# Kernel tuning notes

Measured on AMD Instinct MI355X. Metric: run time of the kernel, lower is better.

## Reference

```python
import jax, jax.numpy as jnp
import numpy as np

N_EMBD = 768
N_EXP = 8
DIM_HIDDEN = int(N_EMBD * 4 * 2 / 3)  # 2048
B = 8
CAP = 1024


def setup_inputs() -> dict:
    key = jax.random.key(0)
    k1, k2, k3 = jax.random.split(key, 3)
    std_fc = N_EXP ** (-0.5)  # matches torch init: dim = c_fc.shape[0] = n_exp
    x = jax.random.normal(k1, (B, N_EXP, CAP, N_EMBD), dtype=jnp.float32)
    c_fc = jax.random.uniform(k2, (N_EXP, N_EMBD, 2 * DIM_HIDDEN), dtype=jnp.float32,
                              minval=-std_fc, maxval=std_fc)
    c_proj = jax.random.uniform(k3, (N_EXP, DIM_HIDDEN, N_EMBD), dtype=jnp.float32,
                                minval=-std_fc, maxval=std_fc)
    gamma = jnp.ones((N_EMBD,), dtype=jnp.float32)       # RMSNorm gamma
    mult_bias = jnp.ones((DIM_HIDDEN,), dtype=jnp.float32)  # GEGLU mult_bias
    return {"x": x, "c_fc": c_fc, "c_proj": c_proj, "gamma": gamma, "mult_bias": mult_bias}


def _moe_forward(x, c_fc, c_proj, gamma, mult_bias):
    # x: [b, e, n, d] -> [e, b, n, d]
    h = jnp.transpose(x, (1, 0, 2, 3))
    # RMSNorm (prenorm): F.normalize(x, dim=-1) * gamma * sqrt(d)
    scale = N_EMBD ** 0.5
    l2 = jnp.sqrt(jnp.sum(h * h, axis=-1, keepdims=True))
    h = h / jnp.maximum(l2, 1e-12) * gamma * scale
    # per-expert grouped GEMM: [e,b,n,d] @ [e,d,2h] -> [e,b,n,2h]
    u = jnp.einsum('ebnd,edh->ebnh', h, c_fc)
    # GEGLU: first half is value, second half is gate
    v, gate = u[..., :DIM_HIDDEN], u[..., DIM_HIDDEN:]
    g = jax.nn.gelu(gate, approximate=False) * v * mult_bias
    # project back: [e,b,n,h] @ [e,h,d] -> [e,b,n,d]
    out = jnp.einsum('ebnh,ehd->ebnd', g, c_proj)
    # back to [b, e, n, d]; dropout is identity (p=0.0)
    return jnp.transpose(out, (1, 0, 2, 3))


def reference(x, c_fc, c_proj, gamma, mult_bias):
    return _moe_forward(x, c_fc, c_proj, gamma, mult_bias)
```

## Files before the change

kernel.cpp:

```cpp
#include <hip/hip_runtime.h>
#include <math.h>

#define N_EMBD 768
#define N_EXP  8
#define DIMH   2048
#define CAPN   1024
#define M_TOT  8192

typedef __bf16 bf16x8 __attribute__((ext_vector_type(8)));
typedef float  f32x4  __attribute__((ext_vector_type(4)));
typedef unsigned short u16x4 __attribute__((ext_vector_type(4)));

__device__ __forceinline__ unsigned short f2bf(float f) {
    unsigned int u = __float_as_uint(f);
    unsigned int r = (u + 0x7fffu + ((u >> 16) & 1u)) >> 16;
    return (unsigned short)r;
}

__device__ __forceinline__ void gload16(const void* g, void* l) {
    __builtin_amdgcn_global_load_lds(
        (const __attribute__((address_space(1))) unsigned int*)g,
        (__attribute__((address_space(3))) unsigned int*)l, 16, 0, 0);
}

__device__ __forceinline__ float gelu_exact(float x) {
    float ax = fabsf(x);
    float z  = ax * 0.70710678118654752f;
    float t  = __builtin_amdgcn_rcpf(fmaf(0.3275911f, z, 1.0f));
    float p  = fmaf(t, 1.061405429f, -1.453152027f);
    p = fmaf(p, t, 1.421413741f);
    p = fmaf(p, t, -0.284496736f);
    p = fmaf(p, t, 0.254829592f);
    p = p * t;
    float ez = __expf(-z * z);
    float erfz = fmaf(-p, ez, 1.0f);
    return 0.5f * fmaf(ax, erfz, x);
}

__global__ __launch_bounds__(256) void norm_convert_kernel(
        const float* __restrict__ x, const float* __restrict__ gamma,
        unsigned short* __restrict__ h) {
    int r = (blockIdx.x << 2) | (threadIdx.x >> 6);
    int lane = threadIdx.x & 63;
    int e = r >> 13, m = r & 8191;
    int b = m >> 10, nc = m & 1023;
    const float4* row = (const float4*)(x + (size_t)((b * N_EXP + e) * CAPN + nc) * N_EMBD);
    const float4* g4  = (const float4*)gamma;

    float4 v0 = row[lane], v1 = row[lane + 64], v2 = row[lane + 128];
    float acc = v0.x*v0.x + v0.y*v0.y + v0.z*v0.z + v0.w*v0.w
              + v1.x*v1.x + v1.y*v1.y + v1.z*v1.z + v1.w*v1.w
              + v2.x*v2.x + v2.y*v2.y + v2.z*v2.z + v2.w*v2.w;
#pragma unroll
    for (int off = 32; off >= 1; off >>= 1) acc += __shfl_xor(acc, off, 64);
    float s = 27.712812921102035f / fmaxf(sqrtf(acc), 1e-12f);

    float4 g0 = g4[lane], g1 = g4[lane + 64], g2 = g4[lane + 128];
    u16x4* o4 = (u16x4*)(h + (size_t)(e * M_TOT + m) * N_EMBD);
    u16x4 o;
    o[0]=f2bf(v0.x*s*g0.x); o[1]=f2bf(v0.y*s*g0.y); o[2]=f2bf(v0.z*s*g0.z); o[3]=f2bf(v0.w*s*g0.w);
    o4[lane] = o;
    o[0]=f2bf(v1.x*s*g1.x); o[1]=f2bf(v1.y*s*g1.y); o[2]=f2bf(v1.z*s*g1.z); o[3]=f2bf(v1.w*s*g1.w);
    o4[lane + 64] = o;
    o[0]=f2bf(v2.x*s*g2.x); o[1]=f2bf(v2.y*s*g2.y); o[2]=f2bf(v2.z*s*g2.z); o[3]=f2bf(v2.w*s*g2.w);
    o4[lane + 128] = o;
}

__global__ __launch_bounds__(256) void transpose_convert_kernel(
        const float* __restrict__ in, unsigned short* __restrict__ out, int R, int C) {
    __shared__ float tile[32][33];
    int c0 = blockIdx.x * 32, r0 = blockIdx.y * 32;
    const float* ip = in + (size_t)blockIdx.z * R * C;
    unsigned short* op = out + (size_t)blockIdx.z * R * C;
    int tx = threadIdx.x & 31, ty = threadIdx.x >> 5;
#pragma unroll
    for (int i = 0; i < 4; ++i)
        tile[ty + 8 * i][tx] = ip[(size_t)(r0 + ty + 8 * i) * C + c0 + tx];
    __syncthreads();
#pragma unroll
    for (int i = 0; i < 4; ++i)
        op[(size_t)(c0 + ty + 8 * i) * R + r0 + tx] = f2bf(tile[tx][ty + 8 * i]);
}

#define SBB  __builtin_amdgcn_s_barrier(); \
             asm volatile("s_waitcnt lgkmcnt(0)" ::: "memory"); \
             __builtin_amdgcn_sched_barrier(0); \
             __builtin_amdgcn_s_setprio(1)
#define SBE  __builtin_amdgcn_s_setprio(0); __builtin_amdgcn_s_barrier()
#define VMW0 do { asm volatile("s_waitcnt vmcnt(0)" ::: "memory"); \
             __builtin_amdgcn_sched_barrier(0); } while (0)

#define STG2(PSRC, RS, KO, DOFF) do { \
    gload16((PSRC) + (size_t)sr * (RS) + (KO) + scs, lds + (DOFF) + ldst); \
    gload16((PSRC) + (size_t)(sr + 64) * (RS) + (KO) + scs, lds + (DOFF) + ldst + 4096); \
  } while (0)

#define RDF(V) (*(const bf16x8*)(lds + (V)))

#define RDA4(AF, DB, IB) do { \
    _Pragma("unroll") for (int i_ = 0; i_ < 4; ++i_) { \
      AF[i_][0] = RDF((DB)*32768 + aB + ((IB) + i_)*1024 + sl0); \
      AF[i_][1] = RDF((DB)*32768 + aB + ((IB) + i_)*1024 + sl1); } \
  } while (0)

#define RDB2(BF, DB, BASE) do { \
    _Pragma("unroll") for (int j_ = 0; j_ < 2; ++j_) { \
      BF[j_][0] = RDF((DB)*32768 + (BASE) + j_*1024 + sl0); \
      BF[j_][1] = RDF((DB)*32768 + (BASE) + j_*1024 + sl1); } \
  } while (0)

#define QUAD(ACC, MS, NB, AF, BF) do { \
    _Pragma("unroll") for (int i_ = 0; i_ < 4; ++i_) \
    _Pragma("unroll") for (int j_ = 0; j_ < 2; ++j_) { \
      ACC[(MS)*4 + i_][(NB) + j_] = __builtin_amdgcn_mfma_f32_16x16x32_bf16( \
          AF[i_][0], BF[j_][0], ACC[(MS)*4 + i_][(NB) + j_], 0, 0, 0); \
      ACC[(MS)*4 + i_][(NB) + j_] = __builtin_amdgcn_mfma_f32_16x16x32_bf16( \
          AF[i_][1], BF[j_][1], ACC[(MS)*4 + i_][(NB) + j_], 0, 0, 0); } \
  } while (0)

__global__ __launch_bounds__(512, 2) void gemm1_kernel(
        const unsigned short* __restrict__ hb,
        const unsigned short* __restrict__ fT,
        const float* __restrict__ mbias,
        unsigned short* __restrict__ gb,
        int e0) {
    __shared__ __align__(16) unsigned short lds[65536];
    const int t = threadIdx.x;
    const int e = e0 + blockIdx.z;
    const int m0 = blockIdx.x * 256;
    const int n0 = blockIdx.y * 128;
    const unsigned short* pA  = hb + ((size_t)e * M_TOT + m0) * N_EMBD;
    const unsigned short* pBv = fT + ((size_t)e * 2 * DIMH + n0) * N_EMBD;
    const unsigned short* pBg = pBv + (size_t)DIMH * N_EMBD;
    unsigned short* pG = gb + (size_t)blockIdx.z * M_TOT * DIMH;

    const int sr   = t >> 3;
    const int scs  = ((t & 7) ^ (sr & 7)) * 8;
    const int ldst = t * 8;
    const int lane = t & 63, lo = lane & 15, quad = lane >> 4;
    const int w = t >> 6, wm = w & 1, wn = w >> 1;
    const int sl0 = ((quad    ) ^ (lo & 7)) * 8;
    const int sl1 = ((quad + 4) ^ (lo & 7)) * 8;
    const int aB  = wm * 8192 + lo * 64;
    const int bvB = 16384 + (wn * 32 + lo) * 64;
    const int bgB = 24576 + (wn * 32 + lo) * 64;

#define STA1(D, H, KO)  STG2(pA + (size_t)(H) * 128 * N_EMBD, N_EMBD, KO, (D)*32768 + (H)*8192)
#define STBV1(D, KO)    STG2(pBv, N_EMBD, KO, (D)*32768 + 16384)
#define STBG1(D, KO)    STG2(pBg, N_EMBD, KO, (D)*32768 + 24576)
#define STALL1(D, KO)   do { STA1(D,0,KO); STA1(D,1,KO); STBV1(D,KO); STBG1(D,KO); } while (0)

    f32x4 accv[8][2], accg[8][2];
#pragma unroll
    for (int i = 0; i < 8; ++i)
#pragma unroll
        for (int j = 0; j < 2; ++j) { accv[i][j] = (f32x4)0.f; accg[i][j] = (f32x4)0.f; }
    bf16x8 a0[4][2], a1[4][2], bv[2][2], bg[2][2];

    STALL1(0, 0);
    VMW0;
    __builtin_amdgcn_s_barrier();

    int ko = 64;
    for (int it = 0; it < 6; ++it) {
        const bool more = (it < 5);
        STALL1(1, ko);
        RDA4(a0, 0, 0); RDB2(bv, 0, bvB);
        SBB; QUAD(accv, 0, 0, a0, bv); SBE;
        RDA4(a1, 0, 4);
        SBB; QUAD(accv, 1, 0, a1, bv); SBE;
        RDB2(bg, 0, bgB);
        SBB; QUAD(accg, 1, 0, a1, bg); SBE;
        VMW0;
        SBB; QUAD(accg, 0, 0, a0, bg); SBE;
        if (more) STALL1(0, ko + 64);
        RDA4(a0, 1, 0); RDB2(bv, 1, bvB);
        SBB; QUAD(accv, 0, 0, a0, bv); SBE;
        RDA4(a1, 1, 4);
        SBB; QUAD(accv, 1, 0, a1, bv); SBE;
        RDB2(bg, 1, bgB);
        SBB; QUAD(accg, 1, 0, a1, bg); SBE;
        VMW0;
        SBB; QUAD(accg, 0, 0, a0, bg); SBE;
        ko += 128;
    }

#pragma unroll
    for (int i = 0; i < 8; ++i) {
        const int mb = m0 + wm * 128 + i * 16 + quad * 4;
#pragma unroll
        for (int j = 0; j < 2; ++j) {
            const int n = n0 + wn * 32 + j * 16 + lo;
            const float mbv = mbias[n];
#pragma unroll
            for (int r = 0; r < 4; ++r) {
                float ge = gelu_exact(accg[i][j][r]);
                pG[(size_t)(mb + r) * DIMH + n] = f2bf(ge * accv[i][j][r] * mbv);
            }
        }
    }
#undef STA1
#undef STBV1
#undef STBG1
#undef STALL1
}

__global__ __launch_bounds__(512, 2) void gemm2_kernel(
        const unsigned short* __restrict__ gb,
        const unsigned short* __restrict__ pT,
        float* __restrict__ out, int e0) {
    __shared__ __align__(16) unsigned short lds[65536];
    const int t = threadIdx.x;
    const int e = e0 + blockIdx.z;
    const int m0 = blockIdx.x * 256;
    const int n0 = blockIdx.y * 256;
    const unsigned short* pA = gb + (size_t)blockIdx.z * M_TOT * DIMH + (size_t)m0 * DIMH;
    const unsigned short* pB = pT + ((size_t)e * N_EMBD + n0) * DIMH;

    const int sr   = t >> 3;
    const int scs  = ((t & 7) ^ (sr & 7)) * 8;
    const int ldst = t * 8;
    const int lane = t & 63, lo = lane & 15, quad = lane >> 4;
    const int w = t >> 6, wm = w & 1, wn = w >> 1;
    const int sl0 = ((quad    ) ^ (lo & 7)) * 8;
    const int sl1 = ((quad + 4) ^ (lo & 7)) * 8;
    const int aB  = wm * 8192 + lo * 64;
    const int bB  = 16384 + (wn >> 1) * 8192 + ((wn & 1) * 64 + lo) * 64;

#define STA2(D, H, KO)  STG2(pA + (size_t)(H) * 128 * DIMH, DIMH, KO, (D)*32768 + (H)*8192)
#define STB2(D, H, KO)  STG2(pB + (size_t)(H) * 128 * DIMH, DIMH, KO, (D)*32768 + 16384 + (H)*8192)
#define STALL2(D, KO)   do { STA2(D,0,KO); STA2(D,1,KO); STB2(D,0,KO); STB2(D,1,KO); } while (0)

    f32x4 acc[8][4];
#pragma unroll
    for (int i = 0; i < 8; ++i)
#pragma unroll
        for (int j = 0; j < 4; ++j) acc[i][j] = (f32x4)0.f;
    bf16x8 a0[4][2], a1[4][2], bb[2][2];

    STALL2(0, 0);
    VMW0;
    __builtin_amdgcn_s_barrier();

    int ko = 64;
    for (int it = 0; it < 16; ++it) {
        const bool more = (it < 15);
        STALL2(1, ko);
        RDA4(a0, 0, 0); RDB2(bb, 0, bB);
        SBB; QUAD(acc, 0, 0, a0, bb); SBE;
        RDA4(a1, 0, 4);
        SBB; QUAD(acc, 1, 0, a1, bb); SBE;
        RDB2(bb, 0, bB + 2048);
        SBB; QUAD(acc, 1, 2, a1, bb); SBE;
        VMW0;
        SBB; QUAD(acc, 0, 2, a0, bb); SBE;
        if (more) STALL2(0, ko + 64);
        RDA4(a0, 1, 0); RDB2(bb, 1, bB);
        SBB; QUAD(acc, 0, 0, a0, bb); SBE;
        RDA4(a1, 1, 4);
        SBB; QUAD(acc, 1, 0, a1, bb); SBE;
        RDB2(bb, 1, bB + 2048);
        SBB; QUAD(acc, 1, 2, a1, bb); SBE;
        VMW0;
        SBB; QUAD(acc, 0, 2, a0, bb); SBE;
        ko += 128;
    }

#pragma unroll
    for (int i = 0; i < 8; ++i) {
        const int mb = m0 + wm * 128 + i * 16 + quad * 4;
#pragma unroll
        for (int r = 0; r < 4; ++r) {
            const int m = mb + r;
            const int b = m >> 10, nc = m & 1023;
            float* orow = out + (size_t)((b * N_EXP + e) * CAPN + nc) * N_EMBD;
#pragma unroll
            for (int j = 0; j < 4; ++j)
                orow[n0 + wn * 64 + j * 16 + lo] = acc[i][j][r];
        }
    }
#undef STA2
#undef STB2
#undef STALL2
}

extern "C" void kernel_launch(void* const* d_in, const int* in_sizes, int n_in,
                              void* d_out, int out_size, void* d_ws, size_t ws_size,
                              hipStream_t stream) {
    const float* x     = (const float*)d_in[0];
    const float* cfc   = (const float*)d_in[1];
    const float* cproj = (const float*)d_in[2];
    const float* gamma = (const float*)d_in[3];
    const float* mbias = (const float*)d_in[4];
    float* out = (float*)d_out;

    unsigned short* h      = (unsigned short*)d_ws;
    unsigned short* cfcT   = h + 50331648ull;
    unsigned short* cprojT = cfcT + 25165824ull;
    unsigned short* gbuf   = cprojT + 12582912ull;
    const size_t need_batched = 444596224ull;

    norm_convert_kernel<<<dim3(N_EXP * M_TOT / 4), dim3(256), 0, stream>>>(x, gamma, h);
    transpose_convert_kernel<<<dim3(2 * DIMH / 32, N_EMBD / 32, N_EXP), dim3(256), 0, stream>>>(
        cfc, cfcT, N_EMBD, 2 * DIMH);
    transpose_convert_kernel<<<dim3(N_EMBD / 32, DIMH / 32, N_EXP), dim3(256), 0, stream>>>(
        cproj, cprojT, DIMH, N_EMBD);

    if (ws_size >= need_batched) {
        gemm1_kernel<<<dim3(M_TOT / 256, DIMH / 128, N_EXP), dim3(512), 0, stream>>>(
            h, cfcT, mbias, gbuf, 0);
        gemm2_kernel<<<dim3(M_TOT / 256, N_EMBD / 256, N_EXP), dim3(512), 0, stream>>>(
            gbuf, cprojT, out, 0);
    } else {
        for (int e = 0; e < N_EXP; ++e) {
            gemm1_kernel<<<dim3(M_TOT / 256, DIMH / 128, 1), dim3(512), 0, stream>>>(
                h, cfcT, mbias, gbuf, e);
            gemm2_kernel<<<dim3(M_TOT / 256, N_EMBD / 256, 1), dim3(512), 0, stream>>>(
                gbuf, cprojT, out, e);
        }
    }
}
```

Measured before the change: 1.196 ms.

## Interleave global-to-LDS loads per sub-tile with partial vmcnt waits in both GEMMs

Both GEMM kernels now issue their global_load_lds prefetches in small pieces spread between the MFMA quads, instead of one bulk stage per half-iteration. They wait with partial vmcnt counts instead of draining every outstanding load. The goal is to hide memory latency and avoid full pipeline drains at each stage boundary. The cost is much tighter correctness reasoning: the vmcnt counts must match issue order exactly, or stale LDS data could be read.

```diff
diff --git a/kernel.cpp b/kernel.cpp
--- a/kernel.cpp
+++ b/kernel.cpp
@@ -87,7 +87,7 @@
              __builtin_amdgcn_sched_barrier(0); \
              __builtin_amdgcn_s_setprio(1)
 #define SBE  __builtin_amdgcn_s_setprio(0); __builtin_amdgcn_s_barrier()
-#define VMW0 do { asm volatile("s_waitcnt vmcnt(0)" ::: "memory"); \
+#define VMW(N) do { asm volatile("s_waitcnt vmcnt(" #N ")" ::: "memory"); \
              __builtin_amdgcn_sched_barrier(0); } while (0)
 
 #define STG2(PSRC, RS, KO, DOFF) do { \
@@ -148,7 +148,6 @@
 #define STA1(D, H, KO)  STG2(pA + (size_t)(H) * 128 * N_EMBD, N_EMBD, KO, (D)*32768 + (H)*8192)
 #define STBV1(D, KO)    STG2(pBv, N_EMBD, KO, (D)*32768 + 16384)
 #define STBG1(D, KO)    STG2(pBg, N_EMBD, KO, (D)*32768 + 24576)
-#define STALL1(D, KO)   do { STA1(D,0,KO); STA1(D,1,KO); STBV1(D,KO); STBG1(D,KO); } while (0)
 
     f32x4 accv[8][2], accg[8][2];
 #pragma unroll
@@ -157,32 +156,39 @@
         for (int j = 0; j < 2; ++j) { accv[i][j] = (f32x4)0.f; accg[i][j] = (f32x4)0.f; }
     bf16x8 a0[4][2], a1[4][2], bv[2][2], bg[2][2];
 
-    STALL1(0, 0);
-    VMW0;
+    STBV1(0, 0); STA1(0, 0, 0); STA1(0, 1, 0); STBG1(0, 0);
+    STBV1(1, 64); STA1(1, 0, 64); STA1(1, 1, 64);
+    VMW(6);
     __builtin_amdgcn_s_barrier();
 
-    int ko = 64;
     for (int it = 0; it < 6; ++it) {
         const bool more = (it < 5);
-        STALL1(1, ko);
+        const int koO  = it * 128 + 64;
+        const int koE2 = it * 128 + 128;
+        const int koO2 = it * 128 + 192;
         RDA4(a0, 0, 0); RDB2(bv, 0, bvB);
+        STBG1(1, koO);
         SBB; QUAD(accv, 0, 0, a0, bv); SBE;
         RDA4(a1, 0, 4);
+        if (more) STBV1(0, koE2);
+        VMW(8);
         SBB; QUAD(accv, 1, 0, a1, bv); SBE;
         RDB2(bg, 0, bgB);
+        if (more) STA1(0, 0, koE2);
         SBB; QUAD(accg, 1, 0, a1, bg); SBE;
-        VMW0;
+        if (more) { STA1(0, 1, koE2); VMW(6); } else { VMW(2); }
         SBB; QUAD(accg, 0, 0, a0, bg); SBE;
-        if (more) STALL1(0, ko + 64);
         RDA4(a0, 1, 0); RDB2(bv, 1, bvB);
+        if (more) STBG1(0, koE2);
         SBB; QUAD(accv, 0, 0, a0, bv); SBE;
         RDA4(a1, 1, 4);
+        if (more) STBV1(1, koO2); else VMW(0);
         SBB; QUAD(accv, 1, 0, a1, bv); SBE;
         RDB2(bg, 1, bgB);
+        if (more) STA1(1, 0, koO2);
         SBB; QUAD(accg, 1, 0, a1, bg); SBE;
-        VMW0;
+        if (more) { STA1(1, 1, koO2); VMW(8); }
         SBB; QUAD(accg, 0, 0, a0, bg); SBE;
-        ko += 128;
     }
 
 #pragma unroll
@@ -202,7 +208,6 @@
 #undef STA1
 #undef STBV1
 #undef STBG1
-#undef STALL1
 }
 
 __global__ __launch_bounds__(512, 2) void gemm2_kernel(
@@ -229,7 +234,6 @@
 
 #define STA2(D, H, KO)  STG2(pA + (size_t)(H) * 128 * DIMH, DIMH, KO, (D)*32768 + (H)*8192)
 #define STB2(D, H, KO)  STG2(pB + (size_t)(H) * 128 * DIMH, DIMH, KO, (D)*32768 + 16384 + (H)*8192)
-#define STALL2(D, KO)   do { STA2(D,0,KO); STA2(D,1,KO); STB2(D,0,KO); STB2(D,1,KO); } while (0)
 
     f32x4 acc[8][4];
 #pragma unroll
@@ -238,32 +242,38 @@
         for (int j = 0; j < 4; ++j) acc[i][j] = (f32x4)0.f;
     bf16x8 a0[4][2], a1[4][2], bb[2][2];
 
-    STALL2(0, 0);
-    VMW0;
+    STA2(0, 0, 0); STA2(0, 1, 0); STB2(0, 0, 0); STB2(0, 1, 0);
+    STA2(1, 0, 64); STA2(1, 1, 64);
+    VMW(4);
     __builtin_amdgcn_s_barrier();
 
-    int ko = 64;
     for (int it = 0; it < 16; ++it) {
         const bool more = (it < 15);
-        STALL2(1, ko);
+        const int koO  = it * 128 + 64;
+        const int koE2 = it * 128 + 128;
+        const int koO2 = it * 128 + 192;
         RDA4(a0, 0, 0); RDB2(bb, 0, bB);
+        STB2(1, 0, koO);
         SBB; QUAD(acc, 0, 0, a0, bb); SBE;
         RDA4(a1, 0, 4);
+        STB2(1, 1, koO);
         SBB; QUAD(acc, 1, 0, a1, bb); SBE;
         RDB2(bb, 0, bB + 2048);
+        if (more) STA2(0, 0, koE2);
         SBB; QUAD(acc, 1, 2, a1, bb); SBE;
-        VMW0;
+        if (more) { STA2(0, 1, koE2); VMW(4); } else { VMW(0); }
         SBB; QUAD(acc, 0, 2, a0, bb); SBE;
-        if (more) STALL2(0, ko + 64);
         RDA4(a0, 1, 0); RDB2(bb, 1, bB);
+        if (more) STB2(0, 0, koE2);
         SBB; QUAD(acc, 0, 0, a0, bb); SBE;
         RDA4(a1, 1, 4);
+        if (more) STB2(0, 1, koE2);
         SBB; QUAD(acc, 1, 0, a1, bb); SBE;
         RDB2(bb, 1, bB + 2048);
+        if (more) STA2(1, 0, koO2);
         SBB; QUAD(acc, 1, 2, a1, bb); SBE;
-        VMW0;
+        if (more) { STA2(1, 1, koO2); VMW(4); }
         SBB; QUAD(acc, 0, 2, a0, bb); SBE;
-        ko += 128;
     }
 
 #pragma unroll
@@ -281,7 +291,6 @@
     }
 #undef STA2
 #undef STB2
-#undef STALL2
 }
 
 extern "C" void kernel_launch(void* const* d_in, const int* in_sizes, int n_in,
```

Result: faster. 1.106 ms (-7.5%).
